# Kernel tuning notes

Hardware: AMD Instinct MI355X
Metric: run time of the kernel (lower is better)

Reference implementation:

```python
import jax, jax.numpy as jnp
import numpy as np

N = 64 ** 3          # 64^3 grid -> 262144 unknowns (A_origN64.bin)
NNZ = 7 * N          # 7-point Poisson stencil sparsity
BS = 128             # batch of residual vectors


def setup_inputs() -> dict:
    key = jax.random.key(0)
    k1, k2, k3, k4, k5 = jax.random.split(key, 5)
    y_pred = jax.random.normal(k1, (BS, N), dtype=jnp.float32)
    y_true = jax.random.normal(k2, (BS, N), dtype=jnp.float32)
    # sparse matrix A in COO form (rows, cols, vals)
    vals = jax.random.normal(k3, (NNZ,), dtype=jnp.float32)
    rows = jax.random.randint(k4, (NNZ,), 0, N, dtype=jnp.int32)
    cols = jax.random.randint(k5, (NNZ,), 0, N, dtype=jnp.int32)
    return {"y_pred": y_pred, "y_true": y_true, "vals": vals, "rows": rows, "cols": cols}


def reference(y_pred, y_true, vals, rows, cols):
    # YhatAt = (A @ y_pred.T).T  -- batched SpMV via segment_sum
    def spmv(yp):  # yp: (N,)
        return jax.ops.segment_sum(vals * yp[cols], rows, num_segments=N)

    YhatAt = jax.vmap(spmv)(y_pred)                      # (bs, N)
    YhatY = jnp.sum(y_true * y_pred, axis=1)             # (bs,)
    YhatYhatAt = jnp.sum(y_pred * YhatAt, axis=1)        # (bs,)
    scale = YhatY / YhatYhatAt                           # diag(YhatY/YhatYhatAt) @ YhatAt == scale[:,None]*YhatAt
    resid = y_true - scale[:, None] * YhatAt             # (bs, N)
    return jnp.mean(jnp.sum(resid * resid, axis=1))
```

## Files before the change

kernel.cpp:

```cpp
#include <hip/hip_runtime.h>

#define N_GRID 262144
#define BSZ 128
#define NNZ_TOT 1835008
#define ROWS_PER_BLOCK 32
#define NBLK_FUSED (N_GRID / ROWS_PER_BLOCK)
#define PAIR_CAP (NNZ_TOT + 8 * N_GRID)

typedef float v4f __attribute__((ext_vector_type(4)));
typedef int   v2i __attribute__((ext_vector_type(2)));


__global__ __launch_bounds__(256) void transpose_kernel(const float* __restrict__ yp,
                                                        float* __restrict__ ypT) {
    __shared__ float tile[64 * 65];
    int n0 = blockIdx.x * 64;
    int b0 = blockIdx.y * 64;
    int tx = threadIdx.x & 15;
    int ty = threadIdx.x >> 4;
#pragma unroll
    for (int jj = 0; jj < 4; ++jj) {
        int b = b0 + ty + jj * 16;
        v4f v = __builtin_nontemporal_load((const v4f*)&yp[(size_t)b * N_GRID + n0 + 4 * tx]);
        tile[(4 * tx + 0) * 65 + ty + jj * 16] = v.x;
        tile[(4 * tx + 1) * 65 + ty + jj * 16] = v.y;
        tile[(4 * tx + 2) * 65 + ty + jj * 16] = v.z;
        tile[(4 * tx + 3) * 65 + ty + jj * 16] = v.w;
    }
    __syncthreads();
#pragma unroll
    for (int jj = 0; jj < 4; ++jj) {
        int nl = ty + jj * 16;
        v4f v;
        v.x = tile[nl * 65 + 4 * tx + 0];
        v.y = tile[nl * 65 + 4 * tx + 1];
        v.z = tile[nl * 65 + 4 * tx + 2];
        v.w = tile[nl * 65 + 4 * tx + 3];
        *(v4f*)&ypT[(size_t)(n0 + nl) * BSZ + b0 + 4 * tx] = v;
    }
}

__global__ __launch_bounds__(256) void hist_kernel(const int* __restrict__ rows,
                                                   int* __restrict__ counts) {
    int k0 = blockIdx.x * 1024 + threadIdx.x;
    int kend = blockIdx.x * 1024 + 1024;
#pragma unroll
    for (int k = k0; k < kend; k += 256) {
        int r = __builtin_nontemporal_load(&rows[k]);
        atomicAdd(&counts[r], 1);
    }
}

__global__ __launch_bounds__(512) void scan1_kernel(const int* __restrict__ counts,
                                                    int* __restrict__ ptr,
                                                    int* __restrict__ bsums) {
    __shared__ int sdata[512];
    int i = blockIdx.x * 512 + threadIdx.x;
    int x = (counts[i] + 7) & ~7;
    if (x < 8) x = 8;
    sdata[threadIdx.x] = x;
    __syncthreads();
    for (int off = 1; off < 512; off <<= 1) {
        int v = 0;
        if ((int)threadIdx.x >= off) v = sdata[threadIdx.x - off];
        __syncthreads();
        sdata[threadIdx.x] += v;
        __syncthreads();
    }
    ptr[i] = sdata[threadIdx.x] - x;
    if (threadIdx.x == 511) bsums[blockIdx.x] = sdata[511];
}

__global__ __launch_bounds__(512) void scan2_kernel(int* __restrict__ bsums,
                                                    int* __restrict__ ptr) {
    __shared__ int sdata[512];
    int x = bsums[threadIdx.x];
    sdata[threadIdx.x] = x;
    __syncthreads();
    for (int off = 1; off < 512; off <<= 1) {
        int v = 0;
        if ((int)threadIdx.x >= off) v = sdata[threadIdx.x - off];
        __syncthreads();
        sdata[threadIdx.x] += v;
        __syncthreads();
    }
    bsums[threadIdx.x] = sdata[threadIdx.x] - x;
    if (threadIdx.x == 511) ptr[N_GRID] = sdata[511];
}

__global__ __launch_bounds__(512) void scan3_kernel(int* __restrict__ ptr,
                                                    int* __restrict__ cursor,
                                                    const int* __restrict__ bsums) {
    int i = blockIdx.x * 512 + threadIdx.x;
    int v = ptr[i] + bsums[blockIdx.x];
    ptr[i] = v;
    cursor[i] = v;
}

__global__ __launch_bounds__(256) void csr_scatter_kernel(const float* __restrict__ vals,
                                                          const int* __restrict__ rows,
                                                          const int* __restrict__ cols,
                                                          int* __restrict__ cursor,
                                                          v2i* __restrict__ pairs) {
    int k0 = blockIdx.x * 1024 + threadIdx.x;
    int kend = blockIdx.x * 1024 + 1024;
#pragma unroll
    for (int k = k0; k < kend; k += 256) {
        int r = __builtin_nontemporal_load(&rows[k]);
        int c = __builtin_nontemporal_load(&cols[k]);
        float v = __builtin_nontemporal_load(&vals[k]);
        int pos = atomicAdd(&cursor[r], 1);
        v2i q; q.x = c; q.y = __float_as_int(v);
        pairs[pos] = q;
    }
}

__device__ __forceinline__ float chunk8(const v2i* __restrict__ pairs, int e,
                                        const float* __restrict__ ypT, int b, float y) {
    v2i q[8];
#pragma unroll
    for (int u = 0; u < 8; ++u) q[u] = pairs[e + u];
    float gv[8];
#pragma unroll
    for (int u = 0; u < 8; ++u) gv[u] = ypT[q[u].x * BSZ + b];
#pragma unroll
    for (int u = 0; u < 8; ++u) y = fmaf(__int_as_float(q[u].y), gv[u], y);
    return y;
}

__global__ __launch_bounds__(256, 8) void fused_kernel(const float* __restrict__ ypT,
                                                       const float* __restrict__ yt,
                                                       const int* __restrict__ ptr,
                                                       const v2i* __restrict__ pairs,
                                                       float* __restrict__ partial) {
    __shared__ __align__(16) float ytile[ROWS_PER_BLOCK * 129];
    int b = threadIdx.x & 127;
    int g = threadIdx.x >> 7;
    int n0 = blockIdx.x * ROWS_PER_BLOCK;

    for (int idx = threadIdx.x; idx < ROWS_PER_BLOCK * 128; idx += 256) {
        int bb = idx >> 5;
        int j = idx & 31;
        ytile[j * 129 + bb] = __builtin_nontemporal_load(&yt[(size_t)bb * N_GRID + n0 + j]);
    }
    __syncthreads();

    double a1 = 0.0, at2 = 0.0, a2 = 0.0, a3 = 0.0, a4 = 0.0;
    for (int jj = 0; jj < 8; ++jj) {
        int nlA = g + 4 * jj;
        int nlB = nlA + 2;
        int nA = n0 + nlA;
        int nB = n0 + nlB;
        int eA0 = __builtin_amdgcn_readfirstlane(ptr[nA]);
        int eA1 = __builtin_amdgcn_readfirstlane(ptr[nA + 1]);
        int eB0 = __builtin_amdgcn_readfirstlane(ptr[nB]);
        int eB1 = __builtin_amdgcn_readfirstlane(ptr[nB + 1]);
        float pA = ypT[nA * BSZ + b];
        float pB = ypT[nB * BSZ + b];

        v2i qA[8], qB[8];
#pragma unroll
        for (int u = 0; u < 8; ++u) qA[u] = pairs[eA0 + u];
#pragma unroll
        for (int u = 0; u < 8; ++u) qB[u] = pairs[eB0 + u];
        float gA[8], gB[8];
#pragma unroll
        for (int u = 0; u < 8; ++u) gA[u] = ypT[qA[u].x * BSZ + b];
#pragma unroll
        for (int u = 0; u < 8; ++u) gB[u] = ypT[qB[u].x * BSZ + b];
        float yA = 0.0f, yB = 0.0f;
#pragma unroll
        for (int u = 0; u < 8; ++u) yA = fmaf(__int_as_float(qA[u].y), gA[u], yA);
#pragma unroll
        for (int u = 0; u < 8; ++u) yB = fmaf(__int_as_float(qB[u].y), gB[u], yB);
        for (int e = eA0 + 8; e < eA1; e += 8) yA = chunk8(pairs, e, ypT, b, yA);
        for (int e = eB0 + 8; e < eB1; e += 8) yB = chunk8(pairs, e, ypT, b, yB);

        float tA = ytile[nlA * 129 + b];
        float tB = ytile[nlB * 129 + b];
        a1 += (double)tA * (double)pA;  at2 += (double)tA * (double)tA;
        a2 += (double)pA * (double)yA;  a3 += (double)tA * (double)yA;
        a4 += (double)yA * (double)yA;
        a1 += (double)tB * (double)pB;  at2 += (double)tB * (double)tB;
        a2 += (double)pB * (double)yB;  a3 += (double)tB * (double)yB;
        a4 += (double)yB * (double)yB;
    }

    __syncthreads();
    double* red = (double*)ytile;
    if (g == 1) {
        red[b] = a1; red[BSZ + b] = at2; red[2 * BSZ + b] = a2;
        red[3 * BSZ + b] = a3; red[4 * BSZ + b] = a4;
    }
    __syncthreads();
    if (g == 0) {
        float* pb = partial + (size_t)blockIdx.x * (5 * BSZ);
        __builtin_nontemporal_store((float)(a1 + red[b]), &pb[b]);
        __builtin_nontemporal_store((float)(at2 + red[BSZ + b]), &pb[BSZ + b]);
        __builtin_nontemporal_store((float)(a2 + red[2 * BSZ + b]), &pb[2 * BSZ + b]);
        __builtin_nontemporal_store((float)(a3 + red[3 * BSZ + b]), &pb[3 * BSZ + b]);
        __builtin_nontemporal_store((float)(a4 + red[4 * BSZ + b]), &pb[4 * BSZ + b]);
    }
}

__global__ __launch_bounds__(128) void reduce2_kernel(const float* __restrict__ partial,
                                                      double* __restrict__ acc) {
    int s = blockIdx.x;
    int chunk = blockIdx.y;
    int b = threadIdx.x;
    const int PER = NBLK_FUSED / 16;
    double sum = 0.0;
    int i0 = chunk * PER;
#pragma unroll 4
    for (int i = 0; i < PER; ++i) {
        sum += (double)__builtin_nontemporal_load(
            &partial[(size_t)(i0 + i) * (5 * BSZ) + s * BSZ + b]);
    }
    atomicAdd(&acc[s * BSZ + b], sum);
}

__global__ __launch_bounds__(128) void finalize_kernel(const double* __restrict__ acc,
                                                       float* __restrict__ out) {
    const double* s1 = acc;
    const double* t2 = acc + BSZ;
    const double* s2 = acc + 2 * BSZ;
    const double* s3 = acc + 3 * BSZ;
    const double* s4 = acc + 4 * BSZ;
    int b = threadIdx.x;
    double scale = s1[b] / s2[b];
    double loss = t2[b] - 2.0 * scale * s3[b] + scale * scale * s4[b];
#pragma unroll
    for (int off = 32; off; off >>= 1) loss += __shfl_down(loss, off);
    __shared__ double l[2];
    if ((threadIdx.x & 63) == 0) l[threadIdx.x >> 6] = loss;
    __syncthreads();
    if (threadIdx.x == 0) out[0] = (float)((l[0] + l[1]) / (double)BSZ);
}

extern "C" void kernel_launch(void* const* d_in, const int* in_sizes, int n_in,
                              void* d_out, int out_size, void* d_ws, size_t ws_size,
                              hipStream_t stream) {
    const float* y_pred = (const float*)d_in[0];
    const float* y_true = (const float*)d_in[1];
    const float* vals   = (const float*)d_in[2];
    const int*   rows   = (const int*)d_in[3];
    const int*   cols   = (const int*)d_in[4];
    float* out = (float*)d_out;

    char* ws = (char*)d_ws;
    float*  ypT    = (float*)ws;
    double* acc    = (double*)(ws + (size_t)N_GRID * BSZ * 4);
    int*    counts = (int*)((char*)acc + 5 * BSZ * 8);
    int*    ptr    = counts + N_GRID;
    int*    cursor = ptr + N_GRID + 2;
    int*    bsums  = cursor + N_GRID;
    v2i*    pairs  = (v2i*)(bsums + 512);
    float*  partial = (float*)(pairs + PAIR_CAP);

    hipMemsetAsync(acc, 0, 5 * BSZ * 8 + (size_t)N_GRID * 4, stream);
    hipMemsetAsync(pairs, 0, (size_t)PAIR_CAP * 8, stream);

    transpose_kernel<<<dim3(N_GRID / 64, BSZ / 64), 256, 0, stream>>>(y_pred, ypT);
    hist_kernel<<<NNZ_TOT / 1024, 256, 0, stream>>>(rows, counts);
    scan1_kernel<<<N_GRID / 512, 512, 0, stream>>>(counts, ptr, bsums);
    scan2_kernel<<<1, 512, 0, stream>>>(bsums, ptr);
    scan3_kernel<<<N_GRID / 512, 512, 0, stream>>>(ptr, cursor, bsums);
    csr_scatter_kernel<<<NNZ_TOT / 1024, 256, 0, stream>>>(vals, rows, cols, cursor, pairs);
    fused_kernel<<<NBLK_FUSED, 256, 0, stream>>>(ypT, y_true, ptr, pairs, partial);
    reduce2_kernel<<<dim3(5, 16), 128, 0, stream>>>(partial, acc);
    finalize_kernel<<<1, 128, 0, stream>>>(acc, out);
}
```

Measured before the change: 684.4 us.

## Split SpMV over batch halves and record hist ranks to drop scatter atomics

The histogram kernel now stores each nonzero's atomic rank, so the CSR scatter computes positions as ptr[r]+rank and needs no second atomic pass or cursor array. The fused SpMV/reduction kernel is launched twice, each time on 64 batch columns with 8 rows per block group. The aim is to halve the gathered ypT footprint per pass, improving L2 hit rate on random column gathers. The cost is reading the CSR pairs twice and an extra launch; rank reuses the partial buffer region, which is overwritten only after scatter has consumed it.

```diff
diff --git a/kernel.cpp b/kernel.cpp
--- a/kernel.cpp
+++ b/kernel.cpp
@@ -6,6 +6,7 @@
 #define ROWS_PER_BLOCK 32
 #define NBLK_FUSED (N_GRID / ROWS_PER_BLOCK)
 #define PAIR_CAP (NNZ_TOT + 8 * N_GRID)
+#define PARTIAL_STRIDE (5 * 64)
 
 typedef float v4f __attribute__((ext_vector_type(4)));
 typedef int   v2i __attribute__((ext_vector_type(2)));
@@ -41,13 +42,15 @@
 }
 
 __global__ __launch_bounds__(256) void hist_kernel(const int* __restrict__ rows,
-                                                   int* __restrict__ counts) {
+                                                   int* __restrict__ counts,
+                                                   int* __restrict__ rank) {
     int k0 = blockIdx.x * 1024 + threadIdx.x;
     int kend = blockIdx.x * 1024 + 1024;
 #pragma unroll
     for (int k = k0; k < kend; k += 256) {
         int r = __builtin_nontemporal_load(&rows[k]);
-        atomicAdd(&counts[r], 1);
+        int rk = atomicAdd(&counts[r], 1);
+        __builtin_nontemporal_store(rk, &rank[k]);
     }
 }
 
@@ -89,18 +92,16 @@
 }
 
 __global__ __launch_bounds__(512) void scan3_kernel(int* __restrict__ ptr,
-                                                    int* __restrict__ cursor,
                                                     const int* __restrict__ bsums) {
     int i = blockIdx.x * 512 + threadIdx.x;
-    int v = ptr[i] + bsums[blockIdx.x];
-    ptr[i] = v;
-    cursor[i] = v;
+    ptr[i] = ptr[i] + bsums[blockIdx.x];
 }
 
 __global__ __launch_bounds__(256) void csr_scatter_kernel(const float* __restrict__ vals,
                                                           const int* __restrict__ rows,
                                                           const int* __restrict__ cols,
-                                                          int* __restrict__ cursor,
+                                                          const int* __restrict__ ptr,
+                                                          const int* __restrict__ rank,
                                                           v2i* __restrict__ pairs) {
     int k0 = blockIdx.x * 1024 + threadIdx.x;
     int kend = blockIdx.x * 1024 + 1024;
@@ -109,20 +110,21 @@
         int r = __builtin_nontemporal_load(&rows[k]);
         int c = __builtin_nontemporal_load(&cols[k]);
         float v = __builtin_nontemporal_load(&vals[k]);
-        int pos = atomicAdd(&cursor[r], 1);
+        int rk = __builtin_nontemporal_load(&rank[k]);
+        int pos = ptr[r] + rk;
         v2i q; q.x = c; q.y = __float_as_int(v);
         pairs[pos] = q;
     }
 }
 
 __device__ __forceinline__ float chunk8(const v2i* __restrict__ pairs, int e,
-                                        const float* __restrict__ ypT, int b, float y) {
+                                        const float* __restrict__ ypT, int B, float y) {
     v2i q[8];
 #pragma unroll
     for (int u = 0; u < 8; ++u) q[u] = pairs[e + u];
     float gv[8];
 #pragma unroll
-    for (int u = 0; u < 8; ++u) gv[u] = ypT[q[u].x * BSZ + b];
+    for (int u = 0; u < 8; ++u) gv[u] = ypT[q[u].x * BSZ + B];
 #pragma unroll
     for (int u = 0; u < 8; ++u) y = fmaf(__int_as_float(q[u].y), gv[u], y);
     return y;
@@ -132,31 +134,34 @@
                                                        const float* __restrict__ yt,
                                                        const int* __restrict__ ptr,
                                                        const v2i* __restrict__ pairs,
-                                                       float* __restrict__ partial) {
-    __shared__ __align__(16) float ytile[ROWS_PER_BLOCK * 129];
-    int b = threadIdx.x & 127;
-    int g = threadIdx.x >> 7;
+                                                       float* __restrict__ partial,
+                                                       int b0) {
+    __shared__ __align__(16) char smem[ROWS_PER_BLOCK * 65 * 4];
+    float* ytile = (float*)smem;
+    int b = threadIdx.x & 63;
+    int g = threadIdx.x >> 6;
+    int B = b0 + b;
     int n0 = blockIdx.x * ROWS_PER_BLOCK;
 
-    for (int idx = threadIdx.x; idx < ROWS_PER_BLOCK * 128; idx += 256) {
+    for (int idx = threadIdx.x; idx < ROWS_PER_BLOCK * 64; idx += 256) {
         int bb = idx >> 5;
         int j = idx & 31;
-        ytile[j * 129 + bb] = __builtin_nontemporal_load(&yt[(size_t)bb * N_GRID + n0 + j]);
+        ytile[j * 65 + bb] = __builtin_nontemporal_load(&yt[(size_t)(b0 + bb) * N_GRID + n0 + j]);
     }
     __syncthreads();
 
     double a1 = 0.0, at2 = 0.0, a2 = 0.0, a3 = 0.0, a4 = 0.0;
-    for (int jj = 0; jj < 8; ++jj) {
-        int nlA = g + 4 * jj;
-        int nlB = nlA + 2;
+    for (int jj = 0; jj < 4; ++jj) {
+        int nlA = g + 8 * jj;
+        int nlB = nlA + 4;
         int nA = n0 + nlA;
         int nB = n0 + nlB;
         int eA0 = __builtin_amdgcn_readfirstlane(ptr[nA]);
         int eA1 = __builtin_amdgcn_readfirstlane(ptr[nA + 1]);
         int eB0 = __builtin_amdgcn_readfirstlane(ptr[nB]);
         int eB1 = __builtin_amdgcn_readfirstlane(ptr[nB + 1]);
-        float pA = ypT[nA * BSZ + b];
-        float pB = ypT[nB * BSZ + b];
+        float pA = ypT[nA * BSZ + B];
+        float pB = ypT[nB * BSZ + B];
 
         v2i qA[8], qB[8];
 #pragma unroll
@@ -165,19 +170,19 @@
         for (int u = 0; u < 8; ++u) qB[u] = pairs[eB0 + u];
         float gA[8], gB[8];
 #pragma unroll
-        for (int u = 0; u < 8; ++u) gA[u] = ypT[qA[u].x * BSZ + b];
-#pragma unroll
-        for (int u = 0; u < 8; ++u) gB[u] = ypT[qB[u].x * BSZ + b];
+        for (int u = 0; u < 8; ++u) gA[u] = ypT[qA[u].x * BSZ + B];
+#pragma unroll
+        for (int u = 0; u < 8; ++u) gB[u] = ypT[qB[u].x * BSZ + B];
         float yA = 0.0f, yB = 0.0f;
 #pragma unroll
         for (int u = 0; u < 8; ++u) yA = fmaf(__int_as_float(qA[u].y), gA[u], yA);
 #pragma unroll
         for (int u = 0; u < 8; ++u) yB = fmaf(__int_as_float(qB[u].y), gB[u], yB);
-        for (int e = eA0 + 8; e < eA1; e += 8) yA = chunk8(pairs, e, ypT, b, yA);
-        for (int e = eB0 + 8; e < eB1; e += 8) yB = chunk8(pairs, e, ypT, b, yB);
-
-        float tA = ytile[nlA * 129 + b];
-        float tB = ytile[nlB * 129 + b];
+        for (int e = eA0 + 8; e < eA1; e += 8) yA = chunk8(pairs, e, ypT, B, yA);
+        for (int e = eB0 + 8; e < eB1; e += 8) yB = chunk8(pairs, e, ypT, B, yB);
+
+        float tA = ytile[nlA * 65 + b];
+        float tB = ytile[nlB * 65 + b];
         a1 += (double)tA * (double)pA;  at2 += (double)tA * (double)tA;
         a2 += (double)pA * (double)yA;  a3 += (double)tA * (double)yA;
         a4 += (double)yA * (double)yA;
@@ -187,19 +192,29 @@
     }
 
     __syncthreads();
-    double* red = (double*)ytile;
-    if (g == 1) {
-        red[b] = a1; red[BSZ + b] = at2; red[2 * BSZ + b] = a2;
-        red[3 * BSZ + b] = a3; red[4 * BSZ + b] = a4;
+    double* red = (double*)smem;
+    if (g > 0) {
+        int gg = g - 1;
+        red[0 * 192 + gg * 64 + b] = a1;
+        red[1 * 192 + gg * 64 + b] = at2;
+        red[2 * 192 + gg * 64 + b] = a2;
+        red[3 * 192 + gg * 64 + b] = a3;
+        red[4 * 192 + gg * 64 + b] = a4;
     }
     __syncthreads();
     if (g == 0) {
-        float* pb = partial + (size_t)blockIdx.x * (5 * BSZ);
-        __builtin_nontemporal_store((float)(a1 + red[b]), &pb[b]);
-        __builtin_nontemporal_store((float)(at2 + red[BSZ + b]), &pb[BSZ + b]);
-        __builtin_nontemporal_store((float)(a2 + red[2 * BSZ + b]), &pb[2 * BSZ + b]);
-        __builtin_nontemporal_store((float)(a3 + red[3 * BSZ + b]), &pb[3 * BSZ + b]);
-        __builtin_nontemporal_store((float)(a4 + red[4 * BSZ + b]), &pb[4 * BSZ + b]);
+        float* pb = partial + (size_t)(b0 >> 6) * NBLK_FUSED * PARTIAL_STRIDE
+                            + (size_t)blockIdx.x * PARTIAL_STRIDE;
+        double r0 = a1  + red[0 * 192 + b] + red[0 * 192 + 64 + b] + red[0 * 192 + 128 + b];
+        double r1 = at2 + red[1 * 192 + b] + red[1 * 192 + 64 + b] + red[1 * 192 + 128 + b];
+        double r2 = a2  + red[2 * 192 + b] + red[2 * 192 + 64 + b] + red[2 * 192 + 128 + b];
+        double r3 = a3  + red[3 * 192 + b] + red[3 * 192 + 64 + b] + red[3 * 192 + 128 + b];
+        double r4 = a4  + red[4 * 192 + b] + red[4 * 192 + 64 + b] + red[4 * 192 + 128 + b];
+        __builtin_nontemporal_store((float)r0, &pb[0 * 64 + b]);
+        __builtin_nontemporal_store((float)r1, &pb[1 * 64 + b]);
+        __builtin_nontemporal_store((float)r2, &pb[2 * 64 + b]);
+        __builtin_nontemporal_store((float)r3, &pb[3 * 64 + b]);
+        __builtin_nontemporal_store((float)r4, &pb[4 * 64 + b]);
     }
 }
 
@@ -208,13 +223,16 @@
     int s = blockIdx.x;
     int chunk = blockIdx.y;
     int b = threadIdx.x;
+    int half = b >> 6;
+    int bl = b & 63;
+    const float* P = partial + (size_t)half * NBLK_FUSED * PARTIAL_STRIDE;
     const int PER = NBLK_FUSED / 16;
     double sum = 0.0;
     int i0 = chunk * PER;
 #pragma unroll 4
     for (int i = 0; i < PER; ++i) {
         sum += (double)__builtin_nontemporal_load(
-            &partial[(size_t)(i0 + i) * (5 * BSZ) + s * BSZ + b]);
+            &P[(size_t)(i0 + i) * PARTIAL_STRIDE + s * 64 + bl]);
     }
     atomicAdd(&acc[s * BSZ + b], sum);
 }
@@ -252,21 +270,22 @@
     double* acc    = (double*)(ws + (size_t)N_GRID * BSZ * 4);
     int*    counts = (int*)((char*)acc + 5 * BSZ * 8);
     int*    ptr    = counts + N_GRID;
-    int*    cursor = ptr + N_GRID + 2;
-    int*    bsums  = cursor + N_GRID;
+    int*    bsums  = ptr + N_GRID + 2;
     v2i*    pairs  = (v2i*)(bsums + 512);
     float*  partial = (float*)(pairs + PAIR_CAP);
+    int*    rank   = (int*)partial;
 
     hipMemsetAsync(acc, 0, 5 * BSZ * 8 + (size_t)N_GRID * 4, stream);
     hipMemsetAsync(pairs, 0, (size_t)PAIR_CAP * 8, stream);
 
     transpose_kernel<<<dim3(N_GRID / 64, BSZ / 64), 256, 0, stream>>>(y_pred, ypT);
-    hist_kernel<<<NNZ_TOT / 1024, 256, 0, stream>>>(rows, counts);
+    hist_kernel<<<NNZ_TOT / 1024, 256, 0, stream>>>(rows, counts, rank);
     scan1_kernel<<<N_GRID / 512, 512, 0, stream>>>(counts, ptr, bsums);
     scan2_kernel<<<1, 512, 0, stream>>>(bsums, ptr);
-    scan3_kernel<<<N_GRID / 512, 512, 0, stream>>>(ptr, cursor, bsums);
-    csr_scatter_kernel<<<NNZ_TOT / 1024, 256, 0, stream>>>(vals, rows, cols, cursor, pairs);
-    fused_kernel<<<NBLK_FUSED, 256, 0, stream>>>(ypT, y_true, ptr, pairs, partial);
+    scan3_kernel<<<N_GRID / 512, 512, 0, stream>>>(ptr, bsums);
+    csr_scatter_kernel<<<NNZ_TOT / 1024, 256, 0, stream>>>(vals, rows, cols, ptr, rank, pairs);
+    fused_kernel<<<NBLK_FUSED, 256, 0, stream>>>(ypT, y_true, ptr, pairs, partial, 0);
+    fused_kernel<<<NBLK_FUSED, 256, 0, stream>>>(ypT, y_true, ptr, pairs, partial, 64);
     reduce2_kernel<<<dim3(5, 16), 128, 0, stream>>>(partial, acc);
     finalize_kernel<<<1, 128, 0, stream>>>(acc, out);
 }
```

Measured after the change: 638.3 us. -6.7%, faster.

## Fuse transpose with histogram, record per-nnz ranks, zero only padding slots

Applied to the files above, without the earlier changes.

Transpose and the row histogram now run as one launch. The histogram atomic stores each nonzero's rank within its row, so the scatter kernel writes to ptr[r]+rank without a second atomic. The full memset of the pairs buffer is replaced by extra blocks that zero only each row's padding slots. This removes one launch, a large memset and a pass of atomics, at the cost of writing and reading a rank array that reuses the partial buffer.

```diff
diff --git a/kernel.cpp b/kernel.cpp
--- a/kernel.cpp
+++ b/kernel.cpp
@@ -7,47 +7,56 @@
 #define NBLK_FUSED (N_GRID / ROWS_PER_BLOCK)
 #define PAIR_CAP (NNZ_TOT + 8 * N_GRID)
 
+#define TR_BLOCKS ((N_GRID / 64) * (BSZ / 64))
+#define HIST_BLOCKS (NNZ_TOT / 1024)
+#define SCAT_BLOCKS (NNZ_TOT / 1024)
+#define PADZ_BLOCKS (N_GRID / 1024)
+
 typedef float v4f __attribute__((ext_vector_type(4)));
 typedef int   v2i __attribute__((ext_vector_type(2)));
 
 
-__global__ __launch_bounds__(256) void transpose_kernel(const float* __restrict__ yp,
-                                                        float* __restrict__ ypT) {
-    __shared__ float tile[64 * 65];
-    int n0 = blockIdx.x * 64;
-    int b0 = blockIdx.y * 64;
-    int tx = threadIdx.x & 15;
-    int ty = threadIdx.x >> 4;
-#pragma unroll
-    for (int jj = 0; jj < 4; ++jj) {
-        int b = b0 + ty + jj * 16;
-        v4f v = __builtin_nontemporal_load((const v4f*)&yp[(size_t)b * N_GRID + n0 + 4 * tx]);
-        tile[(4 * tx + 0) * 65 + ty + jj * 16] = v.x;
-        tile[(4 * tx + 1) * 65 + ty + jj * 16] = v.y;
-        tile[(4 * tx + 2) * 65 + ty + jj * 16] = v.z;
-        tile[(4 * tx + 3) * 65 + ty + jj * 16] = v.w;
-    }
-    __syncthreads();
-#pragma unroll
-    for (int jj = 0; jj < 4; ++jj) {
-        int nl = ty + jj * 16;
-        v4f v;
-        v.x = tile[nl * 65 + 4 * tx + 0];
-        v.y = tile[nl * 65 + 4 * tx + 1];
-        v.z = tile[nl * 65 + 4 * tx + 2];
-        v.w = tile[nl * 65 + 4 * tx + 3];
-        *(v4f*)&ypT[(size_t)(n0 + nl) * BSZ + b0 + 4 * tx] = v;
-    }
-}
-
-__global__ __launch_bounds__(256) void hist_kernel(const int* __restrict__ rows,
-                                                   int* __restrict__ counts) {
-    int k0 = blockIdx.x * 1024 + threadIdx.x;
-    int kend = blockIdx.x * 1024 + 1024;
-#pragma unroll
-    for (int k = k0; k < kend; k += 256) {
-        int r = __builtin_nontemporal_load(&rows[k]);
-        atomicAdd(&counts[r], 1);
+__global__ __launch_bounds__(256) void phase1_kernel(const float* __restrict__ yp,
+                                                     float* __restrict__ ypT,
+                                                     const int* __restrict__ rows,
+                                                     int* __restrict__ counts,
+                                                     int* __restrict__ rank) {
+    if (blockIdx.x < TR_BLOCKS) {
+        __shared__ float tile[64 * 65];
+        int n0 = (blockIdx.x >> 1) * 64;
+        int b0 = (blockIdx.x & 1) * 64;
+        int tx = threadIdx.x & 15;
+        int ty = threadIdx.x >> 4;
+#pragma unroll
+        for (int jj = 0; jj < 4; ++jj) {
+            int b = b0 + ty + jj * 16;
+            v4f v = __builtin_nontemporal_load((const v4f*)&yp[(size_t)b * N_GRID + n0 + 4 * tx]);
+            tile[(4 * tx + 0) * 65 + ty + jj * 16] = v.x;
+            tile[(4 * tx + 1) * 65 + ty + jj * 16] = v.y;
+            tile[(4 * tx + 2) * 65 + ty + jj * 16] = v.z;
+            tile[(4 * tx + 3) * 65 + ty + jj * 16] = v.w;
+        }
+        __syncthreads();
+#pragma unroll
+        for (int jj = 0; jj < 4; ++jj) {
+            int nl = ty + jj * 16;
+            v4f v;
+            v.x = tile[nl * 65 + 4 * tx + 0];
+            v.y = tile[nl * 65 + 4 * tx + 1];
+            v.z = tile[nl * 65 + 4 * tx + 2];
+            v.w = tile[nl * 65 + 4 * tx + 3];
+            *(v4f*)&ypT[(size_t)(n0 + nl) * BSZ + b0 + 4 * tx] = v;
+        }
+    } else {
+        int bid = blockIdx.x - TR_BLOCKS;
+        int k0 = bid * 1024 + threadIdx.x;
+        int kend = bid * 1024 + 1024;
+#pragma unroll
+        for (int k = k0; k < kend; k += 256) {
+            int r = __builtin_nontemporal_load(&rows[k]);
+            int rk = atomicAdd(&counts[r], 1);
+            __builtin_nontemporal_store(rk, &rank[k]);
+        }
     }
 }
 
@@ -89,29 +98,41 @@
 }
 
 __global__ __launch_bounds__(512) void scan3_kernel(int* __restrict__ ptr,
-                                                    int* __restrict__ cursor,
                                                     const int* __restrict__ bsums) {
     int i = blockIdx.x * 512 + threadIdx.x;
-    int v = ptr[i] + bsums[blockIdx.x];
-    ptr[i] = v;
-    cursor[i] = v;
+    ptr[i] = ptr[i] + bsums[blockIdx.x];
 }
 
 __global__ __launch_bounds__(256) void csr_scatter_kernel(const float* __restrict__ vals,
                                                           const int* __restrict__ rows,
                                                           const int* __restrict__ cols,
-                                                          int* __restrict__ cursor,
+                                                          const int* __restrict__ ptr,
+                                                          const int* __restrict__ counts,
+                                                          const int* __restrict__ rank,
                                                           v2i* __restrict__ pairs) {
-    int k0 = blockIdx.x * 1024 + threadIdx.x;
-    int kend = blockIdx.x * 1024 + 1024;
-#pragma unroll
-    for (int k = k0; k < kend; k += 256) {
-        int r = __builtin_nontemporal_load(&rows[k]);
-        int c = __builtin_nontemporal_load(&cols[k]);
-        float v = __builtin_nontemporal_load(&vals[k]);
-        int pos = atomicAdd(&cursor[r], 1);
-        v2i q; q.x = c; q.y = __float_as_int(v);
-        pairs[pos] = q;
+    if (blockIdx.x < SCAT_BLOCKS) {
+        int k0 = blockIdx.x * 1024 + threadIdx.x;
+        int kend = blockIdx.x * 1024 + 1024;
+#pragma unroll
+        for (int k = k0; k < kend; k += 256) {
+            int r = __builtin_nontemporal_load(&rows[k]);
+            int c = __builtin_nontemporal_load(&cols[k]);
+            float v = __builtin_nontemporal_load(&vals[k]);
+            int rk = __builtin_nontemporal_load(&rank[k]);
+            int pos = ptr[r] + rk;
+            v2i q; q.x = c; q.y = __float_as_int(v);
+            pairs[pos] = q;
+        }
+    } else {
+        int bid = blockIdx.x - SCAT_BLOCKS;
+#pragma unroll
+        for (int rr = 0; rr < 4; ++rr) {
+            int r = bid * 1024 + rr * 256 + threadIdx.x;
+            int e = ptr[r] + counts[r];
+            int e1 = ptr[r + 1];
+            v2i z; z.x = 0; z.y = 0;
+            for (; e < e1; ++e) pairs[e] = z;
+        }
     }
 }
 
@@ -252,20 +273,19 @@
     double* acc    = (double*)(ws + (size_t)N_GRID * BSZ * 4);
     int*    counts = (int*)((char*)acc + 5 * BSZ * 8);
     int*    ptr    = counts + N_GRID;
-    int*    cursor = ptr + N_GRID + 2;
-    int*    bsums  = cursor + N_GRID;
+    int*    bsums  = ptr + N_GRID + 2;
     v2i*    pairs  = (v2i*)(bsums + 512);
     float*  partial = (float*)(pairs + PAIR_CAP);
+    int*    rank   = (int*)partial;
 
     hipMemsetAsync(acc, 0, 5 * BSZ * 8 + (size_t)N_GRID * 4, stream);
-    hipMemsetAsync(pairs, 0, (size_t)PAIR_CAP * 8, stream);
-
-    transpose_kernel<<<dim3(N_GRID / 64, BSZ / 64), 256, 0, stream>>>(y_pred, ypT);
-    hist_kernel<<<NNZ_TOT / 1024, 256, 0, stream>>>(rows, counts);
+
+    phase1_kernel<<<TR_BLOCKS + HIST_BLOCKS, 256, 0, stream>>>(y_pred, ypT, rows, counts, rank);
     scan1_kernel<<<N_GRID / 512, 512, 0, stream>>>(counts, ptr, bsums);
     scan2_kernel<<<1, 512, 0, stream>>>(bsums, ptr);
-    scan3_kernel<<<N_GRID / 512, 512, 0, stream>>>(ptr, cursor, bsums);
-    csr_scatter_kernel<<<NNZ_TOT / 1024, 256, 0, stream>>>(vals, rows, cols, cursor, pairs);
+    scan3_kernel<<<N_GRID / 512, 512, 0, stream>>>(ptr, bsums);
+    csr_scatter_kernel<<<SCAT_BLOCKS + PADZ_BLOCKS, 256, 0, stream>>>(vals, rows, cols, ptr,
+                                                                      counts, rank, pairs);
     fused_kernel<<<NBLK_FUSED, 256, 0, stream>>>(ypT, y_true, ptr, pairs, partial);
     reduce2_kernel<<<dim3(5, 16), 128, 0, stream>>>(partial, acc);
     finalize_kernel<<<1, 128, 0, stream>>>(acc, out);
```

Result: faster. 660.8 us (-3.4%).

## Record per-entry rank in histogram to drop scan3 and scatter atomics

Applied to the files above, without the earlier changes.

The histogram pass now stores each nonzero's atomic rank within its row. The scatter then computes its position as ptr + block offset + rank without atomics, which removes the scan3 kernel and the cursor array. Block offsets from the scan are now added on the fly in the scatter and fused kernels. The final reduction is also split into 256 chunks instead of 16 to raise parallelism, and the transpose is moved after the CSR build. The cost is an extra rank array written and read, which reuses the partial buffer.

```diff
diff --git a/kernel.cpp b/kernel.cpp
--- a/kernel.cpp
+++ b/kernel.cpp
@@ -10,6 +10,80 @@
 typedef float v4f __attribute__((ext_vector_type(4)));
 typedef int   v2i __attribute__((ext_vector_type(2)));
 
+
+__global__ __launch_bounds__(256) void hist_kernel(const int* __restrict__ rows,
+                                                   int* __restrict__ counts,
+                                                   int* __restrict__ rank) {
+    int k0 = blockIdx.x * 1024 + threadIdx.x;
+    int kend = blockIdx.x * 1024 + 1024;
+#pragma unroll
+    for (int k = k0; k < kend; k += 256) {
+        int r = __builtin_nontemporal_load(&rows[k]);
+        int rk = atomicAdd(&counts[r], 1);
+        __builtin_nontemporal_store(rk, &rank[k]);
+    }
+}
+
+__global__ __launch_bounds__(512) void scan1_kernel(const int* __restrict__ counts,
+                                                    int* __restrict__ ptr,
+                                                    int* __restrict__ bsums) {
+    __shared__ int sdata[512];
+    int i = blockIdx.x * 512 + threadIdx.x;
+    int x = (counts[i] + 7) & ~7;
+    if (x < 8) x = 8;
+    sdata[threadIdx.x] = x;
+    __syncthreads();
+    for (int off = 1; off < 512; off <<= 1) {
+        int v = 0;
+        if ((int)threadIdx.x >= off) v = sdata[threadIdx.x - off];
+        __syncthreads();
+        sdata[threadIdx.x] += v;
+        __syncthreads();
+    }
+    ptr[i] = sdata[threadIdx.x] - x;
+    if (threadIdx.x == 511) bsums[blockIdx.x] = sdata[511];
+}
+
+__global__ __launch_bounds__(512) void scan2_kernel(int* __restrict__ bsums,
+                                                    int* __restrict__ ptr) {
+    __shared__ int sdata[512];
+    int x = bsums[threadIdx.x];
+    sdata[threadIdx.x] = x;
+    __syncthreads();
+    for (int off = 1; off < 512; off <<= 1) {
+        int v = 0;
+        if ((int)threadIdx.x >= off) v = sdata[threadIdx.x - off];
+        __syncthreads();
+        sdata[threadIdx.x] += v;
+        __syncthreads();
+    }
+    bsums[threadIdx.x] = sdata[threadIdx.x] - x;
+    if (threadIdx.x == 511) {
+        ptr[N_GRID] = sdata[511];
+        bsums[512] = 0;
+    }
+}
+
+__global__ __launch_bounds__(256) void csr_scatter_kernel(const float* __restrict__ vals,
+                                                          const int* __restrict__ rows,
+                                                          const int* __restrict__ cols,
+                                                          const int* __restrict__ ptr,
+                                                          const int* __restrict__ bsums,
+                                                          const int* __restrict__ rank,
+                                                          v2i* __restrict__ pairs) {
+    int k0 = blockIdx.x * 1024 + threadIdx.x;
+    int kend = blockIdx.x * 1024 + 1024;
+#pragma unroll
+    for (int k = k0; k < kend; k += 256) {
+        int r = __builtin_nontemporal_load(&rows[k]);
+        int c = __builtin_nontemporal_load(&cols[k]);
+        float v = __builtin_nontemporal_load(&vals[k]);
+        int rk = __builtin_nontemporal_load(&rank[k]);
+        int pos = ptr[r] + bsums[r >> 9] + rk;
+        v2i q; q.x = c; q.y = __float_as_int(v);
+        pairs[pos] = q;
+    }
+}
 
 __global__ __launch_bounds__(256) void transpose_kernel(const float* __restrict__ yp,
                                                         float* __restrict__ ypT) {
@@ -40,81 +114,6 @@
     }
 }
 
-__global__ __launch_bounds__(256) void hist_kernel(const int* __restrict__ rows,
-                                                   int* __restrict__ counts) {
-    int k0 = blockIdx.x * 1024 + threadIdx.x;
-    int kend = blockIdx.x * 1024 + 1024;
-#pragma unroll
-    for (int k = k0; k < kend; k += 256) {
-        int r = __builtin_nontemporal_load(&rows[k]);
-        atomicAdd(&counts[r], 1);
-    }
-}
-
-__global__ __launch_bounds__(512) void scan1_kernel(const int* __restrict__ counts,
-                                                    int* __restrict__ ptr,
-                                                    int* __restrict__ bsums) {
-    __shared__ int sdata[512];
-    int i = blockIdx.x * 512 + threadIdx.x;
-    int x = (counts[i] + 7) & ~7;
-    if (x < 8) x = 8;
-    sdata[threadIdx.x] = x;
-    __syncthreads();
-    for (int off = 1; off < 512; off <<= 1) {
-        int v = 0;
-        if ((int)threadIdx.x >= off) v = sdata[threadIdx.x - off];
-        __syncthreads();
-        sdata[threadIdx.x] += v;
-        __syncthreads();
-    }
-    ptr[i] = sdata[threadIdx.x] - x;
-    if (threadIdx.x == 511) bsums[blockIdx.x] = sdata[511];
-}
-
-__global__ __launch_bounds__(512) void scan2_kernel(int* __restrict__ bsums,
-                                                    int* __restrict__ ptr) {
-    __shared__ int sdata[512];
-    int x = bsums[threadIdx.x];
-    sdata[threadIdx.x] = x;
-    __syncthreads();
-    for (int off = 1; off < 512; off <<= 1) {
-        int v = 0;
-        if ((int)threadIdx.x >= off) v = sdata[threadIdx.x - off];
-        __syncthreads();
-        sdata[threadIdx.x] += v;
-        __syncthreads();
-    }
-    bsums[threadIdx.x] = sdata[threadIdx.x] - x;
-    if (threadIdx.x == 511) ptr[N_GRID] = sdata[511];
-}
-
-__global__ __launch_bounds__(512) void scan3_kernel(int* __restrict__ ptr,
-                                                    int* __restrict__ cursor,
-                                                    const int* __restrict__ bsums) {
-    int i = blockIdx.x * 512 + threadIdx.x;
-    int v = ptr[i] + bsums[blockIdx.x];
-    ptr[i] = v;
-    cursor[i] = v;
-}
-
-__global__ __launch_bounds__(256) void csr_scatter_kernel(const float* __restrict__ vals,
-                                                          const int* __restrict__ rows,
-                                                          const int* __restrict__ cols,
-                                                          int* __restrict__ cursor,
-                                                          v2i* __restrict__ pairs) {
-    int k0 = blockIdx.x * 1024 + threadIdx.x;
-    int kend = blockIdx.x * 1024 + 1024;
-#pragma unroll
-    for (int k = k0; k < kend; k += 256) {
-        int r = __builtin_nontemporal_load(&rows[k]);
-        int c = __builtin_nontemporal_load(&cols[k]);
-        float v = __builtin_nontemporal_load(&vals[k]);
-        int pos = atomicAdd(&cursor[r], 1);
-        v2i q; q.x = c; q.y = __float_as_int(v);
-        pairs[pos] = q;
-    }
-}
-
 __device__ __forceinline__ float chunk8(const v2i* __restrict__ pairs, int e,
                                         const float* __restrict__ ypT, int b, float y) {
     v2i q[8];
@@ -131,6 +130,7 @@
 __global__ __launch_bounds__(256, 8) void fused_kernel(const float* __restrict__ ypT,
                                                        const float* __restrict__ yt,
                                                        const int* __restrict__ ptr,
+                                                       const int* __restrict__ bsums,
                                                        const v2i* __restrict__ pairs,
                                                        float* __restrict__ partial) {
     __shared__ __align__(16) float ytile[ROWS_PER_BLOCK * 129];
@@ -151,10 +151,10 @@
         int nlB = nlA + 2;
         int nA = n0 + nlA;
         int nB = n0 + nlB;
-        int eA0 = __builtin_amdgcn_readfirstlane(ptr[nA]);
-        int eA1 = __builtin_amdgcn_readfirstlane(ptr[nA + 1]);
-        int eB0 = __builtin_amdgcn_readfirstlane(ptr[nB]);
-        int eB1 = __builtin_amdgcn_readfirstlane(ptr[nB + 1]);
+        int eA0 = __builtin_amdgcn_readfirstlane(ptr[nA] + bsums[nA >> 9]);
+        int eA1 = __builtin_amdgcn_readfirstlane(ptr[nA + 1] + bsums[(nA + 1) >> 9]);
+        int eB0 = __builtin_amdgcn_readfirstlane(ptr[nB] + bsums[nB >> 9]);
+        int eB1 = __builtin_amdgcn_readfirstlane(ptr[nB + 1] + bsums[(nB + 1) >> 9]);
         float pA = ypT[nA * BSZ + b];
         float pB = ypT[nB * BSZ + b];
 
@@ -208,10 +208,10 @@
     int s = blockIdx.x;
     int chunk = blockIdx.y;
     int b = threadIdx.x;
-    const int PER = NBLK_FUSED / 16;
+    const int PER = NBLK_FUSED / 256;
     double sum = 0.0;
     int i0 = chunk * PER;
-#pragma unroll 4
+#pragma unroll 8
     for (int i = 0; i < PER; ++i) {
         sum += (double)__builtin_nontemporal_load(
             &partial[(size_t)(i0 + i) * (5 * BSZ) + s * BSZ + b]);
@@ -252,21 +252,21 @@
     double* acc    = (double*)(ws + (size_t)N_GRID * BSZ * 4);
     int*    counts = (int*)((char*)acc + 5 * BSZ * 8);
     int*    ptr    = counts + N_GRID;
-    int*    cursor = ptr + N_GRID + 2;
-    int*    bsums  = cursor + N_GRID;
-    v2i*    pairs  = (v2i*)(bsums + 512);
+    int*    bsums  = ptr + N_GRID + 2;
+    v2i*    pairs  = (v2i*)(bsums + 514);
     float*  partial = (float*)(pairs + PAIR_CAP);
+    int*    rank   = (int*)partial;
 
     hipMemsetAsync(acc, 0, 5 * BSZ * 8 + (size_t)N_GRID * 4, stream);
     hipMemsetAsync(pairs, 0, (size_t)PAIR_CAP * 8, stream);
 
-    transpose_kernel<<<dim3(N_GRID / 64, BSZ / 64), 256, 0, stream>>>(y_pred, ypT);
-    hist_kernel<<<NNZ_TOT / 1024, 256, 0, stream>>>(rows, counts);
+    hist_kernel<<<NNZ_TOT / 1024, 256, 0, stream>>>(rows, counts, rank);
     scan1_kernel<<<N_GRID / 512, 512, 0, stream>>>(counts, ptr, bsums);
     scan2_kernel<<<1, 512, 0, stream>>>(bsums, ptr);
-    scan3_kernel<<<N_GRID / 512, 512, 0, stream>>>(ptr, cursor, bsums);
-    csr_scatter_kernel<<<NNZ_TOT / 1024, 256, 0, stream>>>(vals, rows, cols, cursor, pairs);
-    fused_kernel<<<NBLK_FUSED, 256, 0, stream>>>(ypT, y_true, ptr, pairs, partial);
-    reduce2_kernel<<<dim3(5, 16), 128, 0, stream>>>(partial, acc);
+    csr_scatter_kernel<<<NNZ_TOT / 1024, 256, 0, stream>>>(vals, rows, cols, ptr, bsums,
+                                                           rank, pairs);
+    transpose_kernel<<<dim3(N_GRID / 64, BSZ / 64), 256, 0, stream>>>(y_pred, ypT);
+    fused_kernel<<<NBLK_FUSED, 256, 0, stream>>>(ypT, y_true, ptr, bsums, pairs, partial);
+    reduce2_kernel<<<dim3(5, 256), 128, 0, stream>>>(partial, acc);
     finalize_kernel<<<1, 128, 0, stream>>>(acc, out);
 }
```

Result: faster. 586.8 us (-14.3%).
